# Performance work log

Hardware: AMD Instinct MI355X
Metric: run time of the kernel (lower is better)

## Reference

```python
import jax, jax.numpy as jnp
import numpy as np

B, H, W, HID, K = 8, 48, 48, 64, 3


def _conv(x, w, b):
    # NHWC 'same' conv, stride 1
    return jax.lax.conv_general_dilated(
        x, w, window_strides=(1, 1), padding='SAME',
        dimension_numbers=('NHWC', 'HWIO', 'NHWC')) + b


def setup_inputs() -> dict:
    key = jax.random.key(0)
    ks = jax.random.split(key, 10)
    wscale = 0.02

    def wi(k, shape):
        return jax.random.normal(k, shape, jnp.float32) * wscale

    return {
        'h': jax.random.normal(ks[0], (B, H, W, HID), jnp.float32),
        'm': jax.random.normal(ks[1], (B, H, W, HID), jnp.float32),
        'Wq': wi(ks[2], (K, K, HID, HID)), 'bq': jnp.zeros((HID,), jnp.float32),
        'Wk': wi(ks[3], (K, K, HID, HID)), 'bk': jnp.zeros((HID,), jnp.float32),
        'Wk2': wi(ks[4], (K, K, HID, HID)), 'bk2': jnp.zeros((HID,), jnp.float32),
        'Wv': wi(ks[5], (K, K, HID, HID)), 'bv': jnp.zeros((HID,), jnp.float32),
        'Wv2': wi(ks[6], (K, K, HID, HID)), 'bv2': jnp.zeros((HID,), jnp.float32),
        'Wz': wi(ks[7], (K, K, 2 * HID, 2 * HID)), 'bz': jnp.zeros((2 * HID,), jnp.float32),
        'Wm': wi(ks[8], (K, K, 3 * HID, 3 * HID)), 'bm': jnp.zeros((3 * HID,), jnp.float32),
    }


def reference(h, m, Wq, bq, Wk, bk, Wk2, bk2, Wv, bv, Wv2, bv2, Wz, bz, Wm, bm):
    b, hh, ww, _ = h.shape
    n = hh * ww  # attention sequence length = H*W

    # conv projections from h
    q_h = _conv(h, Wq, bq).reshape(b, n, HID)   # [B, N, D]
    k_h = _conv(h, Wk, bk).reshape(b, n, HID)
    v_h = _conv(h, Wv, bv).reshape(b, n, HID)

    # attention over h (no 1/sqrt(d) scaling, as in original)
    a_h = jax.nn.softmax(jnp.einsum('bnd,bmd->bnm', q_h, k_h), axis=-1)
    z_h = jnp.einsum('bnm,bmd->bnd', a_h, v_h)

    # conv projections from m, shared query q_h
    k_m = _conv(m, Wk2, bk2).reshape(b, n, HID)
    v_m = _conv(m, Wv2, bv2).reshape(b, n, HID)
    a_m = jax.nn.softmax(jnp.einsum('bnd,bmd->bnm', q_h, k_m), axis=-1)
    z_m = jnp.einsum('bnm,bmd->bnd', a_m, v_m)

    z_h = z_h.reshape(b, hh, ww, HID)
    z_m = z_m.reshape(b, hh, ww, HID)
    w_z = jnp.concatenate([z_h, z_m], axis=-1)          # [B,H,W,2D]
    Z = _conv(w_z, Wz, bz)                               # [B,H,W,2D]

    combined = _conv(jnp.concatenate([Z, h], axis=-1), Wm, bm)  # [B,H,W,3D]
    mo, mg, mi = jnp.split(combined, 3, axis=-1)
    mi = jax.nn.sigmoid(mi)
    new_m = (1.0 - mi) * m + mi * jnp.tanh(mg)
    new_h = jax.nn.sigmoid(mo) * new_m
    return (new_h, new_m)
```

## Files before the change

### kernel.cpp

```cpp
#include <hip/hip_runtime.h>

#define BB 8
#define HH 48
#define WW 48
#define DD 64
#define NSEQ (HH*WW)

typedef unsigned short u16;
typedef unsigned long long u64;
typedef __attribute__((ext_vector_type(8))) short short8;
typedef __attribute__((ext_vector_type(4))) float f32x4;

__device__ __forceinline__ float bf2f(u16 u){ return __uint_as_float(((unsigned)u)<<16); }
__device__ __forceinline__ u16 f2bf(float f){
  unsigned u = __float_as_uint(f);
  return (u16)((u + 0x7fffu + ((u>>16)&1u)) >> 16);
}
__device__ __forceinline__ f32x4 mfma16(short8 a, short8 b, f32x4 c){
  return __builtin_amdgcn_mfma_f32_16x16x32_bf16(a, b, c, 0, 0, 0);
}

struct WtSrcs { const float* src[7]; };
__global__ __launch_bounds__(256) void wtrans_all(WtSrcs s, u16* __restrict__ dst){
  int i = blockIdx.x*256 + threadIdx.x;
  if(i >= 663552) return;
  const float* sp; int local, CI, CO;
  if(i < 184320){ int seg = i/36864; local = i - seg*36864; sp = s.src[seg]; CI = 64; CO = 64; }
  else if(i < 331776){ local = i - 184320; sp = s.src[5]; CI = 128; CO = 128; }
  else { local = i - 331776; sp = s.src[6]; CI = 192; CO = 192; }
  int j    = local & 7;
  int lane = (local >> 3) & 63;
  int blk  = local >> 9;
  int nks  = CI/32;
  int ks   = blk % nks;
  int rem  = blk / nks;
  int cot  = rem % (CO/16);
  int kpos = rem / (CO/16);
  int ci = ks*32 + (lane>>4)*8 + j;
  int co = cot*16 + (lane&15);
  dst[i] = f2bf(sp[((size_t)kpos*CI + ci)*CO + co]);
}

struct ConvPtrs {
  const u16*   W[3];
  const float* bias[3];
  u16*         out[3];
  int          vt[3];
  int          nc;
};

__global__ __launch_bounds__(256) void conv64_mfma(
    const float* __restrict__ in0, const float* __restrict__ in1,
    ConvPtrs p0, ConvPtrs p1){
  const int SP = 72;
  __shared__ u16 lds[3][WW+2][SP];
  const float* in = blockIdx.z ? in1 : in0;
  ConvPtrs p = blockIdx.z ? p1 : p0;
  const int b = blockIdx.x / HH, y = blockIdx.x % HH;
  const int tid  = threadIdx.x;
  const int wave = tid >> 6, lane = tid & 63, g = lane >> 4, col = lane & 15;
  const short8 Z8 = {0,0,0,0,0,0,0,0};

  for(int ky=0; ky<3; ky++){
    int ys = y + ky - 1;
    const int NCH = WW*64/8;
    if(ys < 0 || ys >= HH){
      for(int c8 = tid; c8 < NCH; c8 += 256){
        int px = c8 >> 3, cb = (c8 & 7)*8;
        *(short8*)&lds[ky][px+1][cb] = Z8;
      }
    } else {
      const float* rowp = in + (size_t)(b*HH + ys)*WW*64;
      for(int c8 = tid; c8 < NCH; c8 += 256){
        int px = c8 >> 3, cb = (c8 & 7)*8;
        short8 v;
        #pragma unroll
        for(int j=0;j<8;j++) v[j] = (short)f2bf(rowp[px*64 + cb + j]);
        *(short8*)&lds[ky][px+1][cb] = v;
      }
    }
    for(int c8 = tid; c8 < 16; c8 += 256){
      int which = c8 >> 3; int cb = (c8 & 7)*8;
      *(short8*)&lds[ky][which ? (WW+1) : 0][cb] = Z8;
    }
  }
  __syncthreads();

  const f32x4 zf = {0.f,0.f,0.f,0.f};
  f32x4 acc[3][3];
  #pragma unroll
  for(int mt=0; mt<3; mt++)
    #pragma unroll
    for(int c=0; c<3; c++) acc[mt][c] = zf;

  const int nc = p.nc;
  #pragma unroll
  for(int ky=0; ky<3; ky++)
  #pragma unroll
  for(int kx=0; kx<3; kx++)
  #pragma unroll
  for(int ks=0; ks<2; ks++){
    short8 a[3];
    #pragma unroll
    for(int mt=0; mt<3; mt++)
      a[mt] = *(const short8*)&lds[ky][mt*16 + col + kx][ks*32 + g*8];
    #pragma unroll
    for(int c=0; c<3; c++){
      if(c < nc){
        const u16* wp = p.W[c] + ((((ky*3+kx)*4 + wave)*2 + ks)<<9) + lane*8;
        short8 bfr = *(const short8*)wp;
        #pragma unroll
        for(int mt=0; mt<3; mt++)
          acc[mt][c] = mfma16(a[mt], bfr, acc[mt][c]);
      }
    }
  }

  #pragma unroll
  for(int c=0; c<3; c++){
    if(c >= nc) continue;
    int co = wave*16 + col;
    float bs = p.bias[c][co];
    if(p.vt[c]){
      u16* op = p.out[c] + ((size_t)(b*64 + co))*NSEQ + (size_t)y*WW;
      #pragma unroll
      for(int mt=0; mt<3; mt++){
        int px = mt*16 + g*4;
        u64 pk =  (u64)f2bf(acc[mt][c][0] + bs)
               | ((u64)f2bf(acc[mt][c][1] + bs) << 16)
               | ((u64)f2bf(acc[mt][c][2] + bs) << 32)
               | ((u64)f2bf(acc[mt][c][3] + bs) << 48);
        *(u64*)&op[px] = pk;
      }
    } else {
      u16* op = p.out[c] + ((size_t)(b*HH + y)*WW)*64 + co;
      #pragma unroll
      for(int mt=0; mt<3; mt++)
        #pragma unroll
        for(int r=0; r<4; r++){
          int px = mt*16 + g*4 + r;
          op[(size_t)px*64] = f2bf(acc[mt][c][r] + bs);
        }
    }
  }
}

__global__ __launch_bounds__(256) void attn2_mfma(
    const u16* __restrict__ q,
    const u16* __restrict__ kh, const u16* __restrict__ vhT,
    const u16* __restrict__ km2, const u16* __restrict__ vmT,
    u16* __restrict__ po, u16* __restrict__ pox, float2* __restrict__ ml){
  __shared__ u16 Ks [64*64];
  __shared__ u16 Vts[80*64];
  __shared__ u16 Ps [64*64];
  const int qt = blockIdx.x, b = blockIdx.y;
  const int s = blockIdx.z / 3, ch = blockIdx.z % 3;
  const int tid = threadIdx.x, wave = tid>>6, lane = tid&63;
  const int g = lane>>4, col = lane&15;
  const int strip = wave;
  const size_t NP = (size_t)BB*NSEQ*DD;

  const u16* kk = s ? km2 : kh;
  const u16* vT = s ? vmT : vhT;

  const u16* qp = q + ((size_t)(b*NSEQ + qt*64 + strip*16 + col))*DD;
  short8 aq0 = *(const short8*)&qp[g*8];
  short8 aq1 = *(const short8*)&qp[32 + g*8];

  const int r0a = tid>>3, gr = tid&7, cb0 = gr*8;
  const int r0b = r0a + 32;
  const int stA = r0a*64 + ((gr ^ (r0a&7))<<3);
  const int stB = stA + 32*64;
  const size_t tb  = (size_t)(b*NSEQ)*DD;
  const size_t tbT = (size_t)(b*64)*NSEQ;

  const int cg0 = ((g     ^ (col&7))<<3);
  const int cg1 = (((4+g) ^ (col&7))<<3);

  for(int idx = tid; idx < 16*64; idx += 256) Vts[64*64 + idx] = 0x3F80;

  short8 paK0,paK1,paV0,paV1;
  short8 pbK0,pbK1,pbV0,pbV1;

  const f32x4 zf = {0.f,0.f,0.f,0.f};
  f32x4 o[4];
  #pragma unroll
  for(int nt=0; nt<4; nt++) o[nt] = zf;
  f32x4 ol = zf;

#define BAR() { __builtin_amdgcn_s_barrier(); __builtin_amdgcn_sched_barrier(0); }
#define LWAIT() { asm volatile("s_waitcnt lgkmcnt(0)" ::: "memory"); __builtin_amdgcn_sched_barrier(0); }

#define LOADSET(K0,K1,V0,V1, kt_) {                                        \
    size_t offK0 = tb + (size_t)(kt_)*64*DD + (size_t)r0a*DD + cb0;        \
    size_t offK1 = tb + (size_t)(kt_)*64*DD + (size_t)r0b*DD + cb0;        \
    size_t offV0 = tbT + (size_t)r0a*NSEQ + (size_t)(kt_)*64 + cb0;        \
    size_t offV1 = tbT + (size_t)r0b*NSEQ + (size_t)(kt_)*64 + cb0;        \
    K0 = *(const short8*)&kk[offK0];  K1 = *(const short8*)&kk[offK1];     \
    V0 = *(const short8*)&vT[offV0];  V1 = *(const short8*)&vT[offV1];     \
  }
#define STORESET(K0,K1,V0,V1) {                                            \
    *(short8*)&Ks [stA] = K0;   *(short8*)&Ks [stB] = K1;                  \
    *(short8*)&Vts[stA] = V0;   *(short8*)&Vts[stB] = V1;                  \
  }
#define COMPUTE() {                                                 \
    __builtin_amdgcn_s_setprio(1);                                  \
    f32x4 sv[4];                                                    \
    _Pragma("unroll")                                               \
    for(int nt=0; nt<4; nt++){                                      \
      sv[nt] = zf;                                                  \
      int rowb = (nt*16 + col)*64;                                  \
      short8 bk0 = *(const short8*)&Ks[rowb + cg0];                 \
      sv[nt] = mfma16(aq0, bk0, sv[nt]);                            \
      short8 bk1 = *(const short8*)&Ks[rowb + cg1];                 \
      sv[nt] = mfma16(aq1, bk1, sv[nt]);                            \
    }                                                               \
    _Pragma("unroll")                                               \
    for(int r=0; r<4; r++){                                         \
      int prow = strip*16 + g*4 + r;                                \
      int pbase = prow*64;                                          \
      _Pragma("unroll")                                             \
      for(int nt=0; nt<4; nt++)                                     \
        Ps[pbase + (((nt*2 + (col>>3)) ^ (prow&7))<<3) + (col&7)] = f2bf(__expf(sv[nt][r])); \
    }                                                               \
    int prowr = strip*16 + col;                                     \
    _Pragma("unroll")                                               \
    for(int ks=0; ks<2; ks++){                                      \
      short8 ap = *(const short8*)&Ps[prowr*64 + (ks ? cg1 : cg0)]; \
      _Pragma("unroll")                                             \
      for(int nt=0; nt<4; nt++){                                    \
        short8 bv = *(const short8*)&Vts[(nt*16 + col)*64 + (ks ? cg1 : cg0)]; \
        o[nt] = mfma16(ap, bv, o[nt]);                              \
      }                                                             \
      short8 b1 = *(const short8*)&Vts[(64 + col)*64 + (ks ? cg1 : cg0)]; \
      ol = mfma16(ap, b1, ol);                                      \
    }                                                               \
    __builtin_amdgcn_s_setprio(0);                                  \
  }

  const int kt0 = ch*12;
  LOADSET(paK0,paK1,paV0,paV1, kt0);
  for(int kt = kt0; kt < kt0+12; kt += 2){
    LOADSET(pbK0,pbK1,pbV0,pbV1, kt+1);
    BAR();
    STORESET(paK0,paK1,paV0,paV1);
    LWAIT();
    BAR();
    COMPUTE();
    if(kt+2 < kt0+12) LOADSET(paK0,paK1,paV0,paV1, kt+2);
    BAR();
    STORESET(pbK0,pbK1,pbV0,pbV1);
    LWAIT();
    BAR();
    COMPUTE();
  }

  const int ridx = s*3 + ch;
  u16* rbase = (ridx < 4) ? (po + (size_t)ridx*NP) : (pox + (size_t)(ridx-4)*NP);
  u16* pb = rbase + ((size_t)(b*NSEQ + qt*64 + strip*16))*DD;
  #pragma unroll
  for(int nt=0; nt<4; nt++)
    #pragma unroll
    for(int r=0; r<4; r++)
      pb[(g*4 + r)*DD + nt*16 + col] = f2bf(o[nt][r]);
  if(col == 0){
    #pragma unroll
    for(int r=0; r<4; r++){
      int qrow = qt*64 + strip*16 + g*4 + r;
      float2 v; v.x = 0.f; v.y = ol[r];
      ml[(size_t)ridx*BB*NSEQ + (size_t)b*NSEQ + qrow] = v;
    }
  }
#undef LOADSET
#undef STORESET
#undef COMPUTE
#undef BAR
#undef LWAIT
}

__global__ __launch_bounds__(256) void attn_combine(u16* po, const u16* __restrict__ pox,
                                                    const float2* __restrict__ ml){
  const size_t NP = (size_t)BB*NSEQ*DD;
  const size_t RORD = (size_t)BB*NSEQ;
  for(size_t e = (size_t)blockIdx.x*256 + threadIdx.x; e < NP; e += (size_t)gridDim.x*256){
    size_t row = e / DD;
    float lh = ml[row].y + ml[RORD + row].y + ml[2*RORD + row].y;
    float lm = ml[3*RORD + row].y + ml[4*RORD + row].y + ml[5*RORD + row].y;
    float oh = bf2f(po[e]) + bf2f(po[NP + e]) + bf2f(po[2*NP + e]);
    float om = bf2f(po[3*NP + e]) + bf2f(pox[e]) + bf2f(pox[NP + e]);
    po[e]      = f2bf(oh/lh);
    po[NP + e] = f2bf(om/lm);
  }
}

template<int CIN, int COUT, int SPLIT, bool GATE, bool IN1F>
__global__ __launch_bounds__(256) void bigconv_mfma(
    const u16* __restrict__ in0, const u16* __restrict__ in1b, const float* __restrict__ in1f,
    const u16* __restrict__ Wt, const float* __restrict__ bias,
    void* __restrict__ out0v, void* __restrict__ out1v, const float* __restrict__ mem){
  constexpr int SP  = CIN + 8;
  constexpr int NTW = COUT/64;
  __shared__ u16 lds[3][18][SP];
  const int b = blockIdx.x / HH, y = blockIdx.x % HH;
  const int pt = blockIdx.z;
  const int tid  = threadIdx.x;
  const int wave = tid >> 6, lane = tid & 63, g = lane >> 4, col = lane & 15;
  const short8 Z8 = {0,0,0,0,0,0,0,0};

  for(int ky=0; ky<3; ky++){
    int ys = y + ky - 1;
    const int NCH = 18*CIN/8;
    if(ys < 0 || ys >= HH){
      for(int c8 = tid; c8 < NCH; c8 += 256){
        int px = c8 / (CIN/8), cb = (c8 % (CIN/8))*8;
        *(short8*)&lds[ky][px][cb] = Z8;
      }
    } else {
      size_t base0 = (size_t)(b*HH + ys)*WW*SPLIT;
      size_t base1 = (size_t)(b*HH + ys)*WW*(CIN-SPLIT);
      for(int c8 = tid; c8 < NCH; c8 += 256){
        int px = c8 / (CIN/8), cb = (c8 % (CIN/8))*8;
        int x = pt*16 + px - 1;
        short8 val;
        if(x < 0 || x >= WW){
          val = Z8;
        } else if(cb < SPLIT){
          val = *(const short8*)&in0[base0 + (size_t)x*SPLIT + cb];
        } else if constexpr (IN1F){
          const float* sp = &in1f[base1 + (size_t)x*(CIN-SPLIT) + cb - SPLIT];
          #pragma unroll
          for(int j=0;j<8;j++) val[j] = (short)f2bf(sp[j]);
        } else {
          val = *(const short8*)&in1b[base1 + (size_t)x*(CIN-SPLIT) + cb - SPLIT];
        }
        *(short8*)&lds[ky][px][cb] = val;
      }
    }
  }
  __syncthreads();

  const f32x4 zf = {0.f,0.f,0.f,0.f};
  f32x4 acc[NTW];
  #pragma unroll
  for(int i=0; i<NTW; i++) acc[i] = zf;

  #pragma unroll
  for(int ky=0; ky<3; ky++)
  #pragma unroll
  for(int kx=0; kx<3; kx++)
  #pragma unroll
  for(int ks=0; ks<CIN/32; ks++){
    short8 a = *(const short8*)&lds[ky][col + kx][ks*32 + g*8];
    #pragma unroll
    for(int i=0; i<NTW; i++){
      const u16* wp = Wt + (((((ky*3+kx)*(COUT/16)) + (wave + 4*i))*(CIN/32) + ks)<<9) + lane*8;
      short8 bfr = *(const short8*)wp;
      acc[i] = mfma16(a, bfr, acc[i]);
    }
  }

  if constexpr (!GATE){
    u16* out0 = (u16*)out0v;
    #pragma unroll
    for(int i=0; i<NTW; i++){
      int co = (wave + 4*i)*16 + col;
      float bs = bias[co];
      u16* op = out0 + (size_t)(b*HH + y)*WW*COUT + co;
      #pragma unroll
      for(int r=0; r<4; r++){
        int px = pt*16 + g*4 + r;
        op[(size_t)px*COUT] = f2bf(acc[i][r] + bs);
      }
    }
  } else {
    float* oh = (float*)out0v;
    float* om = (float*)out1v;
    int c = wave*16 + col;
    float bo = bias[c], bg = bias[64+c], bgi = bias[128+c];
    #pragma unroll
    for(int r=0; r<4; r++){
      int px = pt*16 + g*4 + r;
      size_t idx = ((size_t)(b*HH + y)*WW + px)*64 + c;
      float mo = acc[0][r] + bo;
      float mg = acc[1][r] + bg;
      float gi = acc[2][r] + bgi;
      float mval = mem[idx];
      float si = 1.f/(1.f + __expf(-gi));
      float nm = (1.f - si)*mval + si*tanhf(mg);
      float nh = (1.f/(1.f + __expf(-mo)))*nm;
      oh[idx] = nh;
      om[idx] = nm;
    }
  }
}

extern "C" void kernel_launch(void* const* d_in, const int* in_sizes, int n_in,
                              void* d_out, int out_size, void* d_ws, size_t ws_size,
                              hipStream_t stream){
  (void)in_sizes; (void)n_in; (void)out_size; (void)ws_size;
  const float* h   = (const float*)d_in[0];
  const float* m   = (const float*)d_in[1];
  const float* Wq  = (const float*)d_in[2];  const float* bq  = (const float*)d_in[3];
  const float* Wk  = (const float*)d_in[4];  const float* bk  = (const float*)d_in[5];
  const float* Wk2 = (const float*)d_in[6];  const float* bk2 = (const float*)d_in[7];
  const float* Wv  = (const float*)d_in[8];  const float* bv  = (const float*)d_in[9];
  const float* Wv2 = (const float*)d_in[10]; const float* bv2 = (const float*)d_in[11];
  const float* Wz  = (const float*)d_in[12]; const float* bz  = (const float*)d_in[13];
  const float* Wm  = (const float*)d_in[14]; const float* bm  = (const float*)d_in[15];

  const size_t NPIX = (size_t)BB*NSEQ*DD;

  u16* ws = (u16*)d_ws;
  u16* WtQ  = ws + 0;
  u16* WtK  = ws + 36864;
  u16* WtK2 = ws + 73728;
  u16* WtV  = ws + 110592;
  u16* WtV2 = ws + 147456;
  u16* WtZ  = ws + 184320;
  u16* WtM  = ws + 331776;
  u16* slotA = ws + 663552;
  u16* slotB = slotA + NPIX;
  u16* slotC = slotB + NPIX;
  u16* slotD = slotC + NPIX;
  u16* slotE = slotD + NPIX;
  u16* pox   = slotE + NPIX;
  float2* ml = (float2*)(pox + 2*NPIX);
  u16* Zb    = slotA;

  float* outh = (float*)d_out;
  float* outm = outh + NPIX;
  u16* po = (u16*)d_out;
  u16* zh = po;
  u16* zm = po + NPIX;

  WtSrcs wsrc;
  wsrc.src[0]=Wq; wsrc.src[1]=Wk; wsrc.src[2]=Wk2; wsrc.src[3]=Wv; wsrc.src[4]=Wv2;
  wsrc.src[5]=Wz; wsrc.src[6]=Wm;
  wtrans_all<<<dim3(2592), 256, 0, stream>>>(wsrc, ws);

  ConvPtrs ph;
  ph.W[0]=WtQ;  ph.W[1]=WtK;  ph.W[2]=WtV;
  ph.bias[0]=bq; ph.bias[1]=bk; ph.bias[2]=bv;
  ph.out[0]=slotA; ph.out[1]=slotB; ph.out[2]=slotC;
  ph.vt[0]=0; ph.vt[1]=0; ph.vt[2]=1;
  ph.nc = 3;

  ConvPtrs pm;
  pm.W[0]=WtK2; pm.W[1]=WtV2; pm.W[2]=WtV2;
  pm.bias[0]=bk2; pm.bias[1]=bv2; pm.bias[2]=bv2;
  pm.out[0]=slotD; pm.out[1]=slotE; pm.out[2]=slotE;
  pm.vt[0]=0; pm.vt[1]=1; pm.vt[2]=1;
  pm.nc = 2;

  conv64_mfma<<<dim3(BB*HH, 1, 2), 256, 0, stream>>>(h, m, ph, pm);

  attn2_mfma<<<dim3(NSEQ/64, BB, 6), 256, 0, stream>>>(
      slotA, slotB, slotC, slotD, slotE, po, pox, ml);

  attn_combine<<<dim3(2048), 256, 0, stream>>>(po, pox, ml);

  bigconv_mfma<128,128,64,false,false><<<dim3(BB*HH, 1, 3), 256, 0, stream>>>(
      zh, zm, (const float*)0, WtZ, bz, (void*)Zb, (void*)0, (const float*)0);

  bigconv_mfma<192,192,128,true,true><<<dim3(BB*HH, 1, 3), 256, 0, stream>>>(
      Zb, (const u16*)0, h, WtM, bm, (void*)outh, (void*)outm, m);
}
```

Baseline: 135.3 us.

## Split conv64 rows into three 16-pixel column tiles for more blocks

The first conv kernel now gives each block a 16-pixel horizontal tile of one row, and the grid's z dimension triples. This raises the block count from 768 to 2304 and shrinks the per-block LDS and accumulator footprint, which should improve occupancy and latency hiding. In exchange, the weight fragments are reloaded from global memory three times as often. Halo columns are also loaded redundantly, and input rows are converted three times.

```diff
diff --git a/kernel.cpp b/kernel.cpp
--- a/kernel.cpp
+++ b/kernel.cpp
@@ -52,10 +52,10 @@
 __global__ __launch_bounds__(256) void conv64_mfma(
     const float* __restrict__ in0, const float* __restrict__ in1,
     ConvPtrs p0, ConvPtrs p1){
-  const int SP = 72;
-  __shared__ u16 lds[3][WW+2][SP];
-  const float* in = blockIdx.z ? in1 : in0;
-  ConvPtrs p = blockIdx.z ? p1 : p0;
+  __shared__ u16 lds[3][18][72];
+  const int sidx = blockIdx.z / 3, pt = blockIdx.z % 3;
+  const float* in = sidx ? in1 : in0;
+  ConvPtrs p = sidx ? p1 : p0;
   const int b = blockIdx.x / HH, y = blockIdx.x % HH;
   const int tid  = threadIdx.x;
   const int wave = tid >> 6, lane = tid & 63, g = lane >> 4, col = lane & 15;
@@ -63,35 +63,33 @@
 
   for(int ky=0; ky<3; ky++){
     int ys = y + ky - 1;
-    const int NCH = WW*64/8;
+    const int NCH = 18*64/8;
     if(ys < 0 || ys >= HH){
       for(int c8 = tid; c8 < NCH; c8 += 256){
         int px = c8 >> 3, cb = (c8 & 7)*8;
-        *(short8*)&lds[ky][px+1][cb] = Z8;
+        *(short8*)&lds[ky][px][cb] = Z8;
       }
     } else {
       const float* rowp = in + (size_t)(b*HH + ys)*WW*64;
       for(int c8 = tid; c8 < NCH; c8 += 256){
         int px = c8 >> 3, cb = (c8 & 7)*8;
+        int x = pt*16 + px - 1;
         short8 v;
-        #pragma unroll
-        for(int j=0;j<8;j++) v[j] = (short)f2bf(rowp[px*64 + cb + j]);
-        *(short8*)&lds[ky][px+1][cb] = v;
-      }
-    }
-    for(int c8 = tid; c8 < 16; c8 += 256){
-      int which = c8 >> 3; int cb = (c8 & 7)*8;
-      *(short8*)&lds[ky][which ? (WW+1) : 0][cb] = Z8;
+        if(x < 0 || x >= WW) v = Z8;
+        else {
+          #pragma unroll
+          for(int j=0;j<8;j++) v[j] = (short)f2bf(rowp[x*64 + cb + j]);
+        }
+        *(short8*)&lds[ky][px][cb] = v;
+      }
     }
   }
   __syncthreads();
 
   const f32x4 zf = {0.f,0.f,0.f,0.f};
-  f32x4 acc[3][3];
-  #pragma unroll
-  for(int mt=0; mt<3; mt++)
-    #pragma unroll
-    for(int c=0; c<3; c++) acc[mt][c] = zf;
+  f32x4 acc[3];
+  #pragma unroll
+  for(int c=0; c<3; c++) acc[c] = zf;
 
   const int nc = p.nc;
   #pragma unroll
@@ -100,18 +98,13 @@
   for(int kx=0; kx<3; kx++)
   #pragma unroll
   for(int ks=0; ks<2; ks++){
-    short8 a[3];
-    #pragma unroll
-    for(int mt=0; mt<3; mt++)
-      a[mt] = *(const short8*)&lds[ky][mt*16 + col + kx][ks*32 + g*8];
+    short8 a = *(const short8*)&lds[ky][col + kx][ks*32 + g*8];
     #pragma unroll
     for(int c=0; c<3; c++){
       if(c < nc){
         const u16* wp = p.W[c] + ((((ky*3+kx)*4 + wave)*2 + ks)<<9) + lane*8;
         short8 bfr = *(const short8*)wp;
-        #pragma unroll
-        for(int mt=0; mt<3; mt++)
-          acc[mt][c] = mfma16(a[mt], bfr, acc[mt][c]);
+        acc[c] = mfma16(a, bfr, acc[c]);
       }
     }
   }
@@ -123,24 +116,19 @@
     float bs = p.bias[c][co];
     if(p.vt[c]){
       u16* op = p.out[c] + ((size_t)(b*64 + co))*NSEQ + (size_t)y*WW;
-      #pragma unroll
-      for(int mt=0; mt<3; mt++){
-        int px = mt*16 + g*4;
-        u64 pk =  (u64)f2bf(acc[mt][c][0] + bs)
-               | ((u64)f2bf(acc[mt][c][1] + bs) << 16)
-               | ((u64)f2bf(acc[mt][c][2] + bs) << 32)
-               | ((u64)f2bf(acc[mt][c][3] + bs) << 48);
-        *(u64*)&op[px] = pk;
-      }
+      int px = pt*16 + g*4;
+      u64 pk =  (u64)f2bf(acc[c][0] + bs)
+             | ((u64)f2bf(acc[c][1] + bs) << 16)
+             | ((u64)f2bf(acc[c][2] + bs) << 32)
+             | ((u64)f2bf(acc[c][3] + bs) << 48);
+      *(u64*)&op[px] = pk;
     } else {
       u16* op = p.out[c] + ((size_t)(b*HH + y)*WW)*64 + co;
       #pragma unroll
-      for(int mt=0; mt<3; mt++)
-        #pragma unroll
-        for(int r=0; r<4; r++){
-          int px = mt*16 + g*4 + r;
-          op[(size_t)px*64] = f2bf(acc[mt][c][r] + bs);
-        }
+      for(int r=0; r<4; r++){
+        int px = pt*16 + g*4 + r;
+        op[(size_t)px*64] = f2bf(acc[c][r] + bs);
+      }
     }
   }
 }
@@ -452,7 +440,7 @@
   pm.vt[0]=0; pm.vt[1]=1; pm.vt[2]=1;
   pm.nc = 2;
 
-  conv64_mfma<<<dim3(BB*HH, 1, 2), 256, 0, stream>>>(h, m, ph, pm);
+  conv64_mfma<<<dim3(BB*HH, 1, 6), 256, 0, stream>>>(h, m, ph, pm);
 
   attn2_mfma<<<dim3(NSEQ/64, BB, 6), 256, 0, stream>>>(
       slotA, slotB, slotC, slotD, slotE, po, pox, ml);
```

Measured after the change: 147.8 us. 9.2% more time.
